# Kernel tuning notes

Measured on AMD Instinct MI355X. Metric: run time of the kernel, lower is better.

## Reference

```python
import jax, jax.numpy as jnp
import numpy as np

H = 256
V = 64
B = 2048
T = 512


def setup_inputs() -> dict:
    key = jax.random.key(0)
    k1, k2, k3 = jax.random.split(key, 3)
    sequential_features = jax.random.normal(k1, (B, T, V), dtype=jnp.float32)
    # kaiming-uniform-like init scale for theta [H, H+V] and theta_dot [1, H]
    bound_t = float(np.sqrt(6.0 / (H + V)))
    theta = jax.random.uniform(k2, (H, H + V), minval=-bound_t, maxval=bound_t, dtype=jnp.float32)
    bound_d = float(np.sqrt(6.0 / H))
    theta_dot = jax.random.uniform(k3, (1, H), minval=-bound_d, maxval=bound_d, dtype=jnp.float32)
    bias = jnp.zeros((1,), dtype=jnp.float32)
    return {"sequential_features": sequential_features, "theta": theta, "bias": bias, "theta_dot": theta_dot}


def reference(sequential_features, theta, bias, theta_dot):
    # sequential_features: [B, T, V]; theta: [H, H+V]; bias: [1]; theta_dot: [1, H]
    Bn = sequential_features.shape[0]
    Hn = theta.shape[0]

    def step(state, token):
        # state: [B, H], token: [B, V]
        st = jnp.concatenate([state, token], axis=1)          # [B, H+V]
        z = st @ theta.T + bias                                # [B, H]
        mean = jnp.mean(z, axis=1, keepdims=True)
        std = jnp.std(z, axis=1, keepdims=True, ddof=1)        # torch.std uses Bessel correction
        z = (z - mean) / std
        return jax.nn.relu(z), None

    xs = jnp.swapaxes(sequential_features, 0, 1)               # [T, B, V]
    init = jnp.zeros((Bn, Hn), dtype=sequential_features.dtype)
    state, _ = jax.lax.scan(step, init, xs)
    logits = jnp.sum(state * theta_dot, axis=1)                # [B]
    return jax.nn.sigmoid(logits)
```

## Files before the change

### kernel.cpp

```cpp
#include <hip/hip_runtime.h>


#define TT 512
#define VV 64
#define HH 256
#define STRD 264

typedef short bf16x8 __attribute__((ext_vector_type(8)));
typedef float f32x4  __attribute__((ext_vector_type(4)));

__device__ __forceinline__ unsigned short f2bf(float f) {
    unsigned int u = __float_as_uint(f);
    return (unsigned short)((u + 0x8000u) >> 16);
}

__device__ __forceinline__ float bf2f(unsigned short u) {
    return __uint_as_float(((unsigned int)u) << 16);
}

__device__ __forceinline__ bf16x8 pack8(float4 a, float4 b) {
    bf16x8 v;
    v[0] = (short)f2bf(a.x); v[1] = (short)f2bf(a.y);
    v[2] = (short)f2bf(a.z); v[3] = (short)f2bf(a.w);
    v[4] = (short)f2bf(b.x); v[5] = (short)f2bf(b.y);
    v[6] = (short)f2bf(b.z); v[7] = (short)f2bf(b.w);
    return v;
}

template <int CTRL>
__device__ __forceinline__ float dppadd(float x) {
    int y = __builtin_amdgcn_update_dpp(0, __float_as_int(x), CTRL, 0xF, 0xF, false);
    return x + __int_as_float(y);
}

template <int CTRL>
__device__ __forceinline__ float dppbcast(float x) {
    int y = __builtin_amdgcn_update_dpp(0, __float_as_int(x), CTRL, 0xF, 0xF, true);
    return __int_as_float(y);
}

__device__ __forceinline__ void barrier_lgkm() {
    asm volatile("s_waitcnt lgkmcnt(0)\n\ts_barrier" ::: "memory");
}

extern "C" __global__ void __launch_bounds__(256, 1)
rnn_scan_kernel(const float* __restrict__ seq,
                const float* __restrict__ theta,
                const float* __restrict__ theta_dot,
                float* __restrict__ out)
{
    __shared__ unsigned short stbuf[2][16][STRD];
    __shared__ __align__(16) float2 partials[64];

    const int tid = threadIdx.x;
    const int w   = tid >> 6;
    const int l   = tid & 63;
    const int q   = l >> 4;
    const int loc = l & 15;
    const int r0  = blockIdx.x << 4;

    bf16x8 bfrag[10][4];
#pragma unroll
    for (int s = 0; s < 4; ++s) {
        const float* trow = theta + (size_t)(w * 64 + s * 16 + loc) * 320;
#pragma unroll
        for (int ks = 0; ks < 10; ++ks) {
            float4 f0 = *(const float4*)(trow + ks * 32 + q * 8);
            float4 f1 = *(const float4*)(trow + ks * 32 + q * 8 + 4);
            bfrag[ks][s] = pack8(f0, f1);
        }
    }

    {
        const int m = tid >> 4, c = (tid & 15) * 16;
        uint4 z = make_uint4(0u, 0u, 0u, 0u);
        *(uint4*)(&stbuf[0][m][c])     = z;
        *(uint4*)(&stbuf[0][m][c + 8]) = z;
    }

    const float* srow = seq + (size_t)(r0 + loc) * (TT * VV);
    float4 tk0 = *(const float4*)(srow + q * 8);
    float4 tk1 = *(const float4*)(srow + q * 8 + 4);
    float4 tk2 = *(const float4*)(srow + 32 + q * 8);
    float4 tk3 = *(const float4*)(srow + 32 + q * 8 + 4);

    __syncthreads();

#pragma unroll 1
    for (int t = 0; t < TT; ++t) {
        unsigned short* stc = &stbuf[t & 1][0][0];
        unsigned short* stn = &stbuf[(t + 1) & 1][0][0];

        bf16x8 a8 = pack8(tk0, tk1);
        bf16x8 a9 = pack8(tk2, tk3);

        if (t + 1 < TT) {
            const float* p = srow + (size_t)(t + 1) * VV;
            tk0 = *(const float4*)(p + q * 8);
            tk1 = *(const float4*)(p + q * 8 + 4);
            tk2 = *(const float4*)(p + 32 + q * 8);
            tk3 = *(const float4*)(p + 32 + q * 8 + 4);
        }

        f32x4 acc[4];
#pragma unroll
        for (int s = 0; s < 4; ++s) { acc[s][0] = 0.f; acc[s][1] = 0.f; acc[s][2] = 0.f; acc[s][3] = 0.f; }

        const unsigned short* arow = stc + loc * STRD;
#pragma unroll
        for (int ks = 0; ks < 8; ++ks) {
            bf16x8 av = *(const bf16x8*)(arow + ks * 32 + q * 8);
#pragma unroll
            for (int s = 0; s < 4; ++s)
                acc[s] = __builtin_amdgcn_mfma_f32_16x16x32_bf16(av, bfrag[ks][s], acc[s], 0, 0, 0);
        }
#pragma unroll
        for (int s = 0; s < 4; ++s)
            acc[s] = __builtin_amdgcn_mfma_f32_16x16x32_bf16(a8, bfrag[8][s], acc[s], 0, 0, 0);
#pragma unroll
        for (int s = 0; s < 4; ++s)
            acc[s] = __builtin_amdgcn_mfma_f32_16x16x32_bf16(a9, bfrag[9][s], acc[s], 0, 0, 0);

        float sum[4], ssq[4];
#pragma unroll
        for (int r = 0; r < 4; ++r) {
            sum[r] = acc[0][r] + acc[1][r] + acc[2][r] + acc[3][r];
            ssq[r] = acc[0][r] * acc[0][r] + acc[1][r] * acc[1][r]
                   + acc[2][r] * acc[2][r] + acc[3][r] * acc[3][r];
        }
#pragma unroll
        for (int r = 0; r < 4; ++r) {
            sum[r] = dppadd<0xB1>(sum[r]);  ssq[r] = dppadd<0xB1>(ssq[r]);
            sum[r] = dppadd<0x4E>(sum[r]);  ssq[r] = dppadd<0x4E>(ssq[r]);
            sum[r] = dppadd<0x124>(sum[r]); ssq[r] = dppadd<0x124>(ssq[r]);
            sum[r] = dppadd<0x128>(sum[r]); ssq[r] = dppadd<0x128>(ssq[r]);
        }
        if (loc < 4)
            partials[((q * 4 + loc) << 2) | w] = make_float2(sum[loc], ssq[loc]);

        barrier_lgkm();

        const int myrow = (q << 2) | (loc & 3);
        float4 pA = *(const float4*)(&partials[myrow << 2]);
        float4 pB = *(const float4*)(&partials[(myrow << 2) | 2]);
        float sumT = (pA.x + pA.z) + (pB.x + pB.z);
        float ssqT = (pA.y + pA.w) + (pB.y + pB.w);
        float mean = sumT * (1.0f / 256.0f);
        float var  = (ssqT - sumT * mean) * (1.0f / 255.0f);
        float rstd = rsqrtf(var);
        float nb   = -mean * rstd;

        float rs[4], nbv[4];
        rs[0] = dppbcast<0x00>(rstd); nbv[0] = dppbcast<0x00>(nb);
        rs[1] = dppbcast<0x55>(rstd); nbv[1] = dppbcast<0x55>(nb);
        rs[2] = dppbcast<0xAA>(rstd); nbv[2] = dppbcast<0xAA>(nb);
        rs[3] = dppbcast<0xFF>(rstd); nbv[3] = dppbcast<0xFF>(nb);

#pragma unroll
        for (int s = 0; s < 4; ++s) {
#pragma unroll
            for (int r = 0; r < 4; ++r) {
                float v = fmaf(acc[s][r], rs[r], nbv[r]);
                v = fmaxf(v, 0.0f);
                stn[(q * 4 + r) * STRD + (w * 64 + s * 16 + loc)] = f2bf(v);
            }
        }
        barrier_lgkm();
    }

    {
        const int m = tid >> 4, c0 = (tid & 15) << 4;
        const unsigned short* sr = &stbuf[0][m][c0];
        float dot = 0.0f;
#pragma unroll
        for (int j = 0; j < 16; ++j)
            dot += bf2f(sr[j]) * theta_dot[c0 + j];
        dot += __shfl_xor(dot, 1, 64);
        dot += __shfl_xor(dot, 2, 64);
        dot += __shfl_xor(dot, 4, 64);
        dot += __shfl_xor(dot, 8, 64);
        if ((tid & 15) == 0)
            out[r0 + m] = 1.0f / (1.0f + expf(-dot));
    }
}

extern "C" void kernel_launch(void* const* d_in, const int* in_sizes, int n_in,
                              void* d_out, int out_size, void* d_ws, size_t ws_size,
                              hipStream_t stream) {
    const float* seq   = (const float*)d_in[0];
    const float* theta = (const float*)d_in[1];
    const float* tdot  = (const float*)d_in[3];
    float* out = (float*)d_out;

    rnn_scan_kernel<<<dim3(128), dim3(256), 0, stream>>>(seq, theta, tdot, out);
}
```

Before: 854.2 us.

## Split hidden dimension across 8 waves per block instead of 4

Doubles the block to 512 threads so each wave computes 32 hidden columns rather than 64, halving the MFMA chain and register-held theta fragments per wave. The cross-wave partial-sum table widens to 8 entries per row, with padding to keep vector reads aligned. This shortens the per-timestep critical path of the serial recurrence at the cost of more barrier participants and a wider reduction.

```diff
diff --git a/kernel.cpp b/kernel.cpp
--- a/kernel.cpp
+++ b/kernel.cpp
@@ -43,14 +43,14 @@
     asm volatile("s_waitcnt lgkmcnt(0)\n\ts_barrier" ::: "memory");
 }
 
-extern "C" __global__ void __launch_bounds__(256, 1)
+extern "C" __global__ void __launch_bounds__(512, 2)
 rnn_scan_kernel(const float* __restrict__ seq,
                 const float* __restrict__ theta,
                 const float* __restrict__ theta_dot,
                 float* __restrict__ out)
 {
     __shared__ unsigned short stbuf[2][16][STRD];
-    __shared__ __align__(16) float2 partials[64];
+    __shared__ __align__(16) float2 partials[16][10];
 
     const int tid = threadIdx.x;
     const int w   = tid >> 6;
@@ -59,10 +59,10 @@
     const int loc = l & 15;
     const int r0  = blockIdx.x << 4;
 
-    bf16x8 bfrag[10][4];
+    bf16x8 bfrag[10][2];
 #pragma unroll
-    for (int s = 0; s < 4; ++s) {
-        const float* trow = theta + (size_t)(w * 64 + s * 16 + loc) * 320;
+    for (int s = 0; s < 2; ++s) {
+        const float* trow = theta + (size_t)(w * 32 + s * 16 + loc) * 320;
 #pragma unroll
         for (int ks = 0; ks < 10; ++ks) {
             float4 f0 = *(const float4*)(trow + ks * 32 + q * 8);
@@ -72,10 +72,9 @@
     }
 
     {
-        const int m = tid >> 4, c = (tid & 15) * 16;
+        const int m = tid >> 5, c = (tid & 31) * 8;
         uint4 z = make_uint4(0u, 0u, 0u, 0u);
-        *(uint4*)(&stbuf[0][m][c])     = z;
-        *(uint4*)(&stbuf[0][m][c + 8]) = z;
+        *(uint4*)(&stbuf[0][m][c]) = z;
     }
 
     const float* srow = seq + (size_t)(r0 + loc) * (TT * VV);
@@ -102,31 +101,27 @@
             tk3 = *(const float4*)(p + 32 + q * 8 + 4);
         }
 
-        f32x4 acc[4];
-#pragma unroll
-        for (int s = 0; s < 4; ++s) { acc[s][0] = 0.f; acc[s][1] = 0.f; acc[s][2] = 0.f; acc[s][3] = 0.f; }
+        f32x4 acc[2];
+        acc[0][0] = 0.f; acc[0][1] = 0.f; acc[0][2] = 0.f; acc[0][3] = 0.f;
+        acc[1][0] = 0.f; acc[1][1] = 0.f; acc[1][2] = 0.f; acc[1][3] = 0.f;
 
         const unsigned short* arow = stc + loc * STRD;
 #pragma unroll
         for (int ks = 0; ks < 8; ++ks) {
             bf16x8 av = *(const bf16x8*)(arow + ks * 32 + q * 8);
-#pragma unroll
-            for (int s = 0; s < 4; ++s)
-                acc[s] = __builtin_amdgcn_mfma_f32_16x16x32_bf16(av, bfrag[ks][s], acc[s], 0, 0, 0);
+            acc[0] = __builtin_amdgcn_mfma_f32_16x16x32_bf16(av, bfrag[ks][0], acc[0], 0, 0, 0);
+            acc[1] = __builtin_amdgcn_mfma_f32_16x16x32_bf16(av, bfrag[ks][1], acc[1], 0, 0, 0);
         }
-#pragma unroll
-        for (int s = 0; s < 4; ++s)
-            acc[s] = __builtin_amdgcn_mfma_f32_16x16x32_bf16(a8, bfrag[8][s], acc[s], 0, 0, 0);
-#pragma unroll
-        for (int s = 0; s < 4; ++s)
-            acc[s] = __builtin_amdgcn_mfma_f32_16x16x32_bf16(a9, bfrag[9][s], acc[s], 0, 0, 0);
+        acc[0] = __builtin_amdgcn_mfma_f32_16x16x32_bf16(a8, bfrag[8][0], acc[0], 0, 0, 0);
+        acc[1] = __builtin_amdgcn_mfma_f32_16x16x32_bf16(a8, bfrag[8][1], acc[1], 0, 0, 0);
+        acc[0] = __builtin_amdgcn_mfma_f32_16x16x32_bf16(a9, bfrag[9][0], acc[0], 0, 0, 0);
+        acc[1] = __builtin_amdgcn_mfma_f32_16x16x32_bf16(a9, bfrag[9][1], acc[1], 0, 0, 0);
 
         float sum[4], ssq[4];
 #pragma unroll
         for (int r = 0; r < 4; ++r) {
-            sum[r] = acc[0][r] + acc[1][r] + acc[2][r] + acc[3][r];
-            ssq[r] = acc[0][r] * acc[0][r] + acc[1][r] * acc[1][r]
-                   + acc[2][r] * acc[2][r] + acc[3][r] * acc[3][r];
+            sum[r] = acc[0][r] + acc[1][r];
+            ssq[r] = acc[0][r] * acc[0][r] + acc[1][r] * acc[1][r];
         }
 #pragma unroll
         for (int r = 0; r < 4; ++r) {
@@ -136,15 +131,17 @@
             sum[r] = dppadd<0x128>(sum[r]); ssq[r] = dppadd<0x128>(ssq[r]);
         }
         if (loc < 4)
-            partials[((q * 4 + loc) << 2) | w] = make_float2(sum[loc], ssq[loc]);
+            partials[q * 4 + loc][w] = make_float2(sum[loc], ssq[loc]);
 
         barrier_lgkm();
 
         const int myrow = (q << 2) | (loc & 3);
-        float4 pA = *(const float4*)(&partials[myrow << 2]);
-        float4 pB = *(const float4*)(&partials[(myrow << 2) | 2]);
-        float sumT = (pA.x + pA.z) + (pB.x + pB.z);
-        float ssqT = (pA.y + pA.w) + (pB.y + pB.w);
+        float4 p0 = *(const float4*)(&partials[myrow][0]);
+        float4 p1 = *(const float4*)(&partials[myrow][2]);
+        float4 p2 = *(const float4*)(&partials[myrow][4]);
+        float4 p3 = *(const float4*)(&partials[myrow][6]);
+        float sumT = ((p0.x + p0.z) + (p1.x + p1.z)) + ((p2.x + p2.z) + (p3.x + p3.z));
+        float ssqT = ((p0.y + p0.w) + (p1.y + p1.w)) + ((p2.y + p2.w) + (p3.y + p3.w));
         float mean = sumT * (1.0f / 256.0f);
         float var  = (ssqT - sumT * mean) * (1.0f / 255.0f);
         float rstd = rsqrtf(var);
@@ -157,18 +154,18 @@
         rs[3] = dppbcast<0xFF>(rstd); nbv[3] = dppbcast<0xFF>(nb);
 
 #pragma unroll
-        for (int s = 0; s < 4; ++s) {
+        for (int s = 0; s < 2; ++s) {
 #pragma unroll
             for (int r = 0; r < 4; ++r) {
                 float v = fmaf(acc[s][r], rs[r], nbv[r]);
                 v = fmaxf(v, 0.0f);
-                stn[(q * 4 + r) * STRD + (w * 64 + s * 16 + loc)] = f2bf(v);
+                stn[(q * 4 + r) * STRD + (w * 32 + s * 16 + loc)] = f2bf(v);
             }
         }
         barrier_lgkm();
     }
 
-    {
+    if (tid < 256) {
         const int m = tid >> 4, c0 = (tid & 15) << 4;
         const unsigned short* sr = &stbuf[0][m][c0];
         float dot = 0.0f;
@@ -192,5 +189,5 @@
     const float* tdot  = (const float*)d_in[3];
     float* out = (float*)d_out;
 
-    rnn_scan_kernel<<<dim3(128), dim3(256), 0, stream>>>(seq, theta, tdot, out);
+    rnn_scan_kernel<<<dim3(128), dim3(512), 0, stream>>>(seq, theta, tdot, out);
 }
```

Measured after the change: 893.1 us. 1.05x slower.

## Fold mean subtraction into centered theta and defer std scaling to next step

Applied to the files above, without the earlier changes.

Subtracts the per-column mean of theta before packing so the matmul output is already zero-mean, removing the row-sum reduction. The per-row std division is deferred: the state is written with the previous step's scale and corrected by rescaling the token input and the final logit. The goal is one barrier per timestep instead of two and fewer DPP reductions. The cost is a theta column-mean pre-pass and different numerics from the rescaling.

```diff
diff --git a/kernel.cpp b/kernel.cpp
--- a/kernel.cpp
+++ b/kernel.cpp
@@ -1,30 +1,30 @@
 #include <hip/hip_runtime.h>
+#include <hip/hip_bf16.h>
 
 
 #define TT 512
 #define VV 64
-#define HH 256
 #define STRD 264
 
 typedef short bf16x8 __attribute__((ext_vector_type(8)));
 typedef float f32x4  __attribute__((ext_vector_type(4)));
 
-__device__ __forceinline__ unsigned short f2bf(float f) {
-    unsigned int u = __float_as_uint(f);
-    return (unsigned short)((u + 0x8000u) >> 16);
-}
-
 __device__ __forceinline__ float bf2f(unsigned short u) {
     return __uint_as_float(((unsigned int)u) << 16);
 }
 
-__device__ __forceinline__ bf16x8 pack8(float4 a, float4 b) {
-    bf16x8 v;
-    v[0] = (short)f2bf(a.x); v[1] = (short)f2bf(a.y);
-    v[2] = (short)f2bf(a.z); v[3] = (short)f2bf(a.w);
-    v[4] = (short)f2bf(b.x); v[5] = (short)f2bf(b.y);
-    v[6] = (short)f2bf(b.z); v[7] = (short)f2bf(b.w);
-    return v;
+__device__ __forceinline__ unsigned int pkbf(float a, float b) {
+    __hip_bfloat162 h = __float22bfloat162_rn(make_float2(a, b));
+    unsigned int u; __builtin_memcpy(&u, &h, 4); return u;
+}
+
+__device__ __forceinline__ bf16x8 pack8s(float4 a, float4 b, float s) {
+    union { bf16x8 v; unsigned int u[4]; } r;
+    r.u[0] = pkbf(a.x * s, a.y * s);
+    r.u[1] = pkbf(a.z * s, a.w * s);
+    r.u[2] = pkbf(b.x * s, b.y * s);
+    r.u[3] = pkbf(b.z * s, b.w * s);
+    return r.v;
 }
 
 template <int CTRL>
@@ -50,7 +50,9 @@
                 float* __restrict__ out)
 {
     __shared__ unsigned short stbuf[2][16][STRD];
-    __shared__ __align__(16) float2 partials[64];
+    __shared__ __align__(16) float partials[2][16][4];
+    __shared__ float cmean[320];
+    __shared__ float dfin[16];
 
     const int tid = threadIdx.x;
     const int w   = tid >> 6;
@@ -59,6 +61,18 @@
     const int loc = l & 15;
     const int r0  = blockIdx.x << 4;
 
+    for (int c = tid; c < 320; c += 256) {
+        float s0 = 0.f, s1 = 0.f, s2 = 0.f, s3 = 0.f;
+        for (int i = 0; i < 256; i += 4) {
+            s0 += theta[(i + 0) * 320 + c];
+            s1 += theta[(i + 1) * 320 + c];
+            s2 += theta[(i + 2) * 320 + c];
+            s3 += theta[(i + 3) * 320 + c];
+        }
+        cmean[c] = ((s0 + s1) + (s2 + s3)) * (1.0f / 256.0f);
+    }
+    __syncthreads();
+
     bf16x8 bfrag[10][4];
 #pragma unroll
     for (int s = 0; s < 4; ++s) {
@@ -67,7 +81,11 @@
         for (int ks = 0; ks < 10; ++ks) {
             float4 f0 = *(const float4*)(trow + ks * 32 + q * 8);
             float4 f1 = *(const float4*)(trow + ks * 32 + q * 8 + 4);
-            bfrag[ks][s] = pack8(f0, f1);
+            float4 c0 = *(const float4*)(&cmean[ks * 32 + q * 8]);
+            float4 c1 = *(const float4*)(&cmean[ks * 32 + q * 8 + 4]);
+            f0.x -= c0.x; f0.y -= c0.y; f0.z -= c0.z; f0.w -= c0.w;
+            f1.x -= c1.x; f1.y -= c1.y; f1.z -= c1.z; f1.w -= c1.w;
+            bfrag[ks][s] = pack8s(f0, f1, 1.0f);
         }
     }
 
@@ -84,15 +102,31 @@
     float4 tk2 = *(const float4*)(srow + 32 + q * 8);
     float4 tk3 = *(const float4*)(srow + 32 + q * 8 + 4);
 
-    __syncthreads();
+    barrier_lgkm();
+
+    float dprev = 1.0f;
 
 #pragma unroll 1
     for (int t = 0; t < TT; ++t) {
         unsigned short* stc = &stbuf[t & 1][0][0];
         unsigned short* stn = &stbuf[(t + 1) & 1][0][0];
 
-        bf16x8 a8 = pack8(tk0, tk1);
-        bf16x8 a9 = pack8(tk2, tk3);
+        float Dtok = 1.0f, g = 1.0f;
+        if (t) {
+            float4 pa = *(const float4*)(&partials[(t + 1) & 1][loc][0]);
+            float dh = sqrtf(((pa.x + pa.y) + (pa.z + pa.w)) * (1.0f / 255.0f));
+            Dtok  = dh * __builtin_amdgcn_rcpf(dprev);
+            dprev = dh;
+            const int wrow = (q << 2) | (l & 3);
+            float4 pb = *(const float4*)(&partials[(t + 1) & 1][wrow][0]);
+            float dw = sqrtf(((pb.x + pb.y) + (pb.z + pb.w)) * (1.0f / 255.0f));
+            g = __builtin_amdgcn_rcpf(dw);
+        }
+        float gr0 = dppbcast<0x00>(g), gr1 = dppbcast<0x55>(g);
+        float gr2 = dppbcast<0xAA>(g), gr3 = dppbcast<0xFF>(g);
+
+        bf16x8 a8 = pack8s(tk0, tk1, Dtok);
+        bf16x8 a9 = pack8s(tk2, tk3, Dtok);
 
         if (t + 1 < TT) {
             const float* p = srow + (size_t)(t + 1) * VV;
@@ -121,52 +155,43 @@
         for (int s = 0; s < 4; ++s)
             acc[s] = __builtin_amdgcn_mfma_f32_16x16x32_bf16(a9, bfrag[9][s], acc[s], 0, 0, 0);
 
-        float sum[4], ssq[4];
+        float ssq[4];
 #pragma unroll
         for (int r = 0; r < 4; ++r) {
-            sum[r] = acc[0][r] + acc[1][r] + acc[2][r] + acc[3][r];
             ssq[r] = acc[0][r] * acc[0][r] + acc[1][r] * acc[1][r]
                    + acc[2][r] * acc[2][r] + acc[3][r] * acc[3][r];
         }
 #pragma unroll
         for (int r = 0; r < 4; ++r) {
-            sum[r] = dppadd<0xB1>(sum[r]);  ssq[r] = dppadd<0xB1>(ssq[r]);
-            sum[r] = dppadd<0x4E>(sum[r]);  ssq[r] = dppadd<0x4E>(ssq[r]);
-            sum[r] = dppadd<0x124>(sum[r]); ssq[r] = dppadd<0x124>(ssq[r]);
-            sum[r] = dppadd<0x128>(sum[r]); ssq[r] = dppadd<0x128>(ssq[r]);
+            ssq[r] = dppadd<0xB1>(ssq[r]);
+            ssq[r] = dppadd<0x4E>(ssq[r]);
+            ssq[r] = dppadd<0x124>(ssq[r]);
+            ssq[r] = dppadd<0x128>(ssq[r]);
         }
         if (loc < 4)
-            partials[((q * 4 + loc) << 2) | w] = make_float2(sum[loc], ssq[loc]);
+            partials[t & 1][q * 4 + loc][w] = ssq[loc];
+
+#pragma unroll
+        for (int s = 0; s < 4; ++s) {
+            const int col = w * 64 + s * 16 + loc;
+            unsigned int u01 = pkbf(fmaxf(acc[s][0], 0.f) * gr0, fmaxf(acc[s][1], 0.f) * gr1);
+            unsigned int u23 = pkbf(fmaxf(acc[s][2], 0.f) * gr2, fmaxf(acc[s][3], 0.f) * gr3);
+            stn[(q * 4 + 0) * STRD + col] = (unsigned short)(u01 & 0xffffu);
+            stn[(q * 4 + 1) * STRD + col] = (unsigned short)(u01 >> 16);
+            stn[(q * 4 + 2) * STRD + col] = (unsigned short)(u23 & 0xffffu);
+            stn[(q * 4 + 3) * STRD + col] = (unsigned short)(u23 >> 16);
+        }
 
         barrier_lgkm();
-
-        const int myrow = (q << 2) | (loc & 3);
-        float4 pA = *(const float4*)(&partials[myrow << 2]);
-        float4 pB = *(const float4*)(&partials[(myrow << 2) | 2]);
-        float sumT = (pA.x + pA.z) + (pB.x + pB.z);
-        float ssqT = (pA.y + pA.w) + (pB.y + pB.w);
-        float mean = sumT * (1.0f / 256.0f);
-        float var  = (ssqT - sumT * mean) * (1.0f / 255.0f);
-        float rstd = rsqrtf(var);
-        float nb   = -mean * rstd;
-
-        float rs[4], nbv[4];
-        rs[0] = dppbcast<0x00>(rstd); nbv[0] = dppbcast<0x00>(nb);
-        rs[1] = dppbcast<0x55>(rstd); nbv[1] = dppbcast<0x55>(nb);
-        rs[2] = dppbcast<0xAA>(rstd); nbv[2] = dppbcast<0xAA>(nb);
-        rs[3] = dppbcast<0xFF>(rstd); nbv[3] = dppbcast<0xFF>(nb);
-
-#pragma unroll
-        for (int s = 0; s < 4; ++s) {
-#pragma unroll
-            for (int r = 0; r < 4; ++r) {
-                float v = fmaf(acc[s][r], rs[r], nbv[r]);
-                v = fmaxf(v, 0.0f);
-                stn[(q * 4 + r) * STRD + (w * 64 + s * 16 + loc)] = f2bf(v);
-            }
-        }
-        barrier_lgkm();
-    }
+    }
+
+    {
+        float4 pa = *(const float4*)(&partials[(TT - 1) & 1][loc][0]);
+        float dh = sqrtf(((pa.x + pa.y) + (pa.z + pa.w)) * (1.0f / 255.0f));
+        float Dfin = dh * __builtin_amdgcn_rcpf(dprev);
+        if (w == 0 && q == 0) dfin[loc] = Dfin;
+    }
+    barrier_lgkm();
 
     {
         const int m = tid >> 4, c0 = (tid & 15) << 4;
@@ -179,8 +204,10 @@
         dot += __shfl_xor(dot, 2, 64);
         dot += __shfl_xor(dot, 4, 64);
         dot += __shfl_xor(dot, 8, 64);
-        if ((tid & 15) == 0)
-            out[r0 + m] = 1.0f / (1.0f + expf(-dot));
+        if ((tid & 15) == 0) {
+            float logit = dot / dfin[m];
+            out[r0 + m] = 1.0f / (1.0f + expf(-logit));
+        }
     }
 }
 
```

Measured after the change: 874.5 us. 1.02x slower.
